# Kernel optimization log

Measured on AMD Instinct MI355X. Metric: run time of the kernel, lower is better.

The kernel has to match this reference:

```python
import jax, jax.numpy as jnp
import numpy as np

# Production-scale sampled 2-hop GraphSAGE flow
N, C, HID, OUT = 1_000_000, 128, 32, 16
NSRC1, NDST1, E1 = 600_000, 80_000, 1_280_000
NDST2, E2 = 8_000, 80_000


def setup_inputs() -> dict:
    key = jax.random.key(0)
    ks = jax.random.split(key, 8)
    x = jax.random.normal(ks[0], (N, C), jnp.float32)
    n_id = jax.random.randint(ks[1], (NSRC1,), 0, N)
    src1 = jax.random.randint(ks[2], (E1,), 0, NSRC1)
    dst1 = jax.random.randint(ks[3], (E1,), 0, NDST1)
    src2 = jax.random.randint(ks[4], (E2,), 0, NDST1)
    dst2 = jax.random.randint(ks[5], (E2,), 0, NDST2)
    W1 = jax.random.normal(ks[6], (C, HID), jnp.float32) / np.sqrt(C).astype(np.float32)
    b1 = jnp.zeros((HID,), jnp.float32)
    W2 = jax.random.normal(ks[7], (HID, OUT), jnp.float32) / np.sqrt(HID).astype(np.float32)
    b2 = jnp.zeros((OUT,), jnp.float32)
    return dict(x=x, n_id=n_id, src1=src1, dst1=dst1, src2=src2, dst2=dst2,
                W1=W1, b1=b1, W2=W2, b2=b2)


def _mean_agg(feat_src, src, dst, num_dst):
    # scatter-mean of source features onto destination nodes (PyG aggr='mean')
    msg = feat_src[src]                                          # [E, F]
    s = jax.ops.segment_sum(msg, dst, num_segments=num_dst)      # [num_dst, F]
    cnt = jax.ops.segment_sum(jnp.ones((src.shape[0],), feat_src.dtype), dst,
                              num_segments=num_dst)
    return s / jnp.maximum(cnt, 1.0)[:, None]


def reference(x, n_id, src1, dst1, src2, dst2, W1, b1, W2, b2):
    h = x[n_id]                                  # gather sampled nodes [NSRC1, C]
    # SAGEConv(concat=False, normalize=False): mean-agg then linear
    h = _mean_agg(h, src1, dst1, NDST1) @ W1 + b1
    h = jax.nn.relu(h)                           # F.dropout(p=0.5) is a no-op in eval
    h = _mean_agg(h, src2, dst2, NDST2) @ W2 + b2
    return jax.nn.log_softmax(h, axis=1)
```

## Files before the change

kernel.cpp:

```cpp
#include <hip/hip_runtime.h>
#include <hip/hip_fp16.h>
#include <math.h>

#define N_NODES  1000000
#define C_IN     128
#define HID      32
#define OUTF     16
#define NSRC1    600000
#define NDST1    80000
#define E1       1280000
#define NDST2    8000
#define E2       80000

#define KB1 4688
#define HB1 5000
#define HB2 313
#define AB1 313
#define AB2 32

#define T1A  1250
#define T1B  (KB1 - T1A)
#define GRP2 1719

#define K1_STRIDE 36

__device__ __forceinline__ void transform_body(
    const float* __restrict__ x, const int* __restrict__ n_id,
    const float* __restrict__ W1, __half* __restrict__ p,
    float* W_s, float (*A_t)[32 * K1_STRIDE], int idx)
{
    for (int i = threadIdx.x; i < C_IN * HID; i += 256) W_s[i] = W1[i];
    __syncthreads();

    const int wave = threadIdx.x >> 6;
    const int lane = threadIdx.x & 63;
    const int gwave = idx * 4 + wave;
    if (gwave >= NSRC1 / 32) return;
    const int s0 = gwave * 32;

    float* At = A_t[wave];

    int   mrow[4]; int f8[4]; const float* rowp[4];
    #pragma unroll
    for (int j = 0; j < 4; ++j) {
        int i2 = j * 64 + lane;
        mrow[j] = i2 >> 3;
        f8[j]   = i2 & 7;
        rowp[j] = x + (size_t)n_id[s0 + mrow[j]] * C_IN + f8[j] * 4;
    }

    const int m4 = lane >> 3;
    const int o4 = lane & 7;

    float acc[4][4];
    #pragma unroll
    for (int i = 0; i < 4; ++i)
        #pragma unroll
        for (int j = 0; j < 4; ++j) acc[i][j] = 0.f;

    float4 v[4];
    #pragma unroll
    for (int j = 0; j < 4; ++j) v[j] = *(const float4*)(rowp[j]);

    #pragma unroll
    for (int c = 0; c < 4; ++c) {
        #pragma unroll
        for (int j = 0; j < 4; ++j) {
            int kb = f8[j] * 4;
            int m  = mrow[j];
            At[(kb + 0) * K1_STRIDE + m] = v[j].x;
            At[(kb + 1) * K1_STRIDE + m] = v[j].y;
            At[(kb + 2) * K1_STRIDE + m] = v[j].z;
            At[(kb + 3) * K1_STRIDE + m] = v[j].w;
        }
        if (c < 3) {
            #pragma unroll
            for (int j = 0; j < 4; ++j)
                v[j] = *(const float4*)(rowp[j] + (c + 1) * 32);
        }
        #pragma unroll 4
        for (int k = 0; k < 32; ++k) {
            float4 a = *(const float4*)&At[k * K1_STRIDE + m4 * 4];
            float4 w = *(const float4*)&W_s[(c * 32 + k) * HID + o4 * 4];
            acc[0][0] += a.x * w.x; acc[0][1] += a.x * w.y; acc[0][2] += a.x * w.z; acc[0][3] += a.x * w.w;
            acc[1][0] += a.y * w.x; acc[1][1] += a.y * w.y; acc[1][2] += a.y * w.z; acc[1][3] += a.y * w.w;
            acc[2][0] += a.z * w.x; acc[2][1] += a.z * w.y; acc[2][2] += a.z * w.z; acc[2][3] += a.z * w.w;
            acc[3][0] += a.w * w.x; acc[3][1] += a.w * w.y; acc[3][2] += a.w * w.z; acc[3][3] += a.w * w.w;
        }
    }

    #pragma unroll
    for (int i = 0; i < 4; ++i) {
        union { __half2 h2[2]; uint2 u; } pk;
        pk.h2[0] = __floats2half2_rn(acc[i][0], acc[i][1]);
        pk.h2[1] = __floats2half2_rn(acc[i][2], acc[i][3]);
        *(uint2*)&p[(size_t)(s0 + m4 * 4 + i) * HID + o4 * 4] = pk.u;
    }
}

__global__ __launch_bounds__(256) void kA1_hist_transform(
    const float* __restrict__ x, const int* __restrict__ n_id,
    const float* __restrict__ W1, __half* __restrict__ p,
    const int* __restrict__ dst1, const int* __restrict__ dst2,
    int* __restrict__ deg1, int* __restrict__ deg2)
{
    __shared__ float W_s[C_IN * HID];
    __shared__ float A_t[4][32 * K1_STRIDE];

    const int bid = blockIdx.x;
    const int t = bid / 5, r = bid % 5;
    if (r == 0 && t < T1A) {
        transform_body(x, n_id, W1, p, W_s, A_t, t);
        return;
    }
    const int nt = min((bid + 4) / 5, T1A);
    const int h  = bid - nt;
    if (h < HB1) {
        int e = h * 256 + threadIdx.x;
        if (e < E1) atomicAdd(&deg1[dst1[e]], 1);
    } else {
        int e = (h - HB1) * 256 + threadIdx.x;
        if (e < E2) atomicAdd(&deg2[dst2[e]], 1);
    }
}

__global__ __launch_bounds__(256) void kB_alloc(
    const int* __restrict__ deg1, const int* __restrict__ deg2,
    int* __restrict__ rs1, int* __restrict__ rs2,
    int* __restrict__ cur1, int* __restrict__ cur2,
    int* __restrict__ counters)
{
    const int bid  = blockIdx.x;
    const int lane = threadIdx.x & 63;
    const int* deg; int* rs; int* cur; int* ctr; int nd; int d;
    if (bid < AB1) { deg = deg1; rs = rs1; cur = cur1; ctr = counters + 0;
                     nd = NDST1; d = bid * 256 + threadIdx.x; }
    else           { deg = deg2; rs = rs2; cur = cur2; ctr = counters + 1;
                     nd = NDST2; d = (bid - AB1) * 256 + threadIdx.x; }

    int v = (d < nd) ? deg[d] : 0;
    int incl = v;
    #pragma unroll
    for (int off = 1; off < 64; off <<= 1) {
        int t = __shfl_up(incl, off, 64);
        if (lane >= off) incl += t;
    }
    int total = __shfl(incl, 63, 64);
    int base = 0;
    if (lane == 63) base = atomicAdd(ctr, total);
    base = __shfl(base, 63, 64);
    if (d < nd) { int r = base + incl - v; rs[d] = r; cur[d] = r; }
}

__global__ __launch_bounds__(256) void kA2_bucket_transform(
    const float* __restrict__ x, const int* __restrict__ n_id,
    const float* __restrict__ W1, __half* __restrict__ p,
    const int* __restrict__ src1, const int* __restrict__ dst1,
    const int* __restrict__ src2, const int* __restrict__ dst2,
    int* __restrict__ cur1, int* __restrict__ cur2,
    int* __restrict__ ss1, int* __restrict__ ss2)
{
    __shared__ float W_s[C_IN * HID];
    __shared__ float A_t[4][32 * K1_STRIDE];

    const int bid = blockIdx.x;
    const int g = bid / 5, r = bid % 5;
    int bidx;
    if (g < GRP2) {
        if (r < 2) {
            int ti = 2 * g + r;
            if (ti < T1B) {
                transform_body(x, n_id, W1, p, W_s, A_t, T1A + ti);
                return;
            }
            bidx = 0;
        } else {
            bidx = 3 * g + (r - 2);
        }
    } else {
        bidx = 3 * GRP2 + (bid - 5 * GRP2);
    }

    if (bidx < HB1) {
        int e = bidx * 256 + threadIdx.x;
        if (e < E1) {
            int d = dst1[e];
            int pos = atomicAdd(&cur1[d], 1);
            ss1[pos] = src1[e];
        }
    } else {
        int e = (bidx - HB1) * 256 + threadIdx.x;
        if (e < E2) {
            int d = dst2[e];
            int pos = atomicAdd(&cur2[d], 1);
            ss2[pos] = src2[e];
        }
    }
}

__global__ __launch_bounds__(256) void kD_gather1(
    const int* __restrict__ row_start, const int* __restrict__ deg,
    const int* __restrict__ ss1, const __half* __restrict__ p,
    const float* __restrict__ b1, const float* __restrict__ W2,
    float* __restrict__ q)
{
    __shared__ float hbuf[16][HID + 1];
    const int g = threadIdx.x >> 4;
    const int f = threadIdx.x & 15;
    const int d = blockIdx.x * 16 + g;

    float w2r[HID];
    #pragma unroll
    for (int k = 0; k < HID; ++k) w2r[k] = W2[k * OUTF + f];
    const float2 b1v = *(const float2*)&b1[2 * f];

    const int start = row_start[d];
    const int dg    = deg[d];
    const __half2* ph2 = (const __half2*)p;

    float2 acc = make_float2(0.f, 0.f);
    int i = 0;
    for (; i + 4 <= dg; i += 4) {
        int s0 = ss1[start + i];
        int s1 = ss1[start + i + 1];
        int s2 = ss1[start + i + 2];
        int s3 = ss1[start + i + 3];
        float2 a = __half22float2(ph2[(size_t)s0 * 16 + f]);
        float2 b = __half22float2(ph2[(size_t)s1 * 16 + f]);
        float2 c = __half22float2(ph2[(size_t)s2 * 16 + f]);
        float2 e = __half22float2(ph2[(size_t)s3 * 16 + f]);
        acc.x += (a.x + b.x) + (c.x + e.x);
        acc.y += (a.y + b.y) + (c.y + e.y);
    }
    for (; i < dg; ++i) {
        float2 a = __half22float2(ph2[(size_t)ss1[start + i] * 16 + f]);
        acc.x += a.x; acc.y += a.y;
    }

    const float inv = 1.f / (float)max(dg, 1);
    hbuf[g][2 * f]     = fmaxf(acc.x * inv + b1v.x, 0.f);
    hbuf[g][2 * f + 1] = fmaxf(acc.y * inv + b1v.y, 0.f);
    float o = 0.f;
    #pragma unroll
    for (int k = 0; k < HID; ++k) o += hbuf[g][k] * w2r[k];
    q[(size_t)d * OUTF + f] = o;
}

__global__ __launch_bounds__(256) void kE_gather2_lsm(
    const int* __restrict__ row_start2, const int* __restrict__ deg2,
    const int* __restrict__ ss2, const float* __restrict__ q,
    const float* __restrict__ b2, float* __restrict__ out)
{
    const int g = threadIdx.x >> 4;
    const int f = threadIdx.x & 15;
    const int d = blockIdx.x * 16 + g;
    if (d >= NDST2) return;

    const int start = row_start2[d];
    const int dg    = deg2[d];

    float acc = 0.f;
    int i = 0;
    for (; i + 2 <= dg; i += 2) {
        int s0 = ss2[start + i];
        int s1 = ss2[start + i + 1];
        acc += q[(size_t)s0 * OUTF + f] + q[(size_t)s1 * OUTF + f];
    }
    if (i < dg) acc += q[(size_t)ss2[start + i] * OUTF + f];

    float z = acc / (float)max(dg, 1) + b2[f];
    float m = z;
    #pragma unroll
    for (int off = 8; off; off >>= 1) m = fmaxf(m, __shfl_xor(m, off, 16));
    float e = expf(z - m);
    float s = e;
    #pragma unroll
    for (int off = 8; off; off >>= 1) s += __shfl_xor(s, off, 16);
    out[(size_t)d * OUTF + f] = z - m - logf(s);
}

extern "C" void kernel_launch(void* const* d_in, const int* in_sizes, int n_in,
                              void* d_out, int out_size, void* d_ws, size_t ws_size,
                              hipStream_t stream)
{
    const float* x    = (const float*)d_in[0];
    const int*   n_id = (const int*)  d_in[1];
    const int*   src1 = (const int*)  d_in[2];
    const int*   dst1 = (const int*)  d_in[3];
    const int*   src2 = (const int*)  d_in[4];
    const int*   dst2 = (const int*)  d_in[5];
    const float* W1   = (const float*)d_in[6];
    const float* b1   = (const float*)d_in[7];
    const float* W2   = (const float*)d_in[8];
    const float* b2   = (const float*)d_in[9];
    float* out = (float*)d_out;

    char* ws = (char*)d_ws;
    __half* p       = (__half*)(ws + 0);
    int*   ss1      = (int*)   (ws + 38400000);
    int*   ss2      = (int*)   (ws + 43520000);
    int*   deg1     = (int*)   (ws + 43840000);
    int*   deg2     = (int*)   (ws + 44160000);
    int*   counters = (int*)   (ws + 44192000);
    int*   rs1      = (int*)   (ws + 44192064);
    int*   rs2      = (int*)   (ws + 44512064);
    int*   cur1     = (int*)   (ws + 44544064);
    int*   cur2     = (int*)   (ws + 44864064);
    float* q        = (float*) (ws + 44896064);

    hipMemsetAsync(deg1, 0, 352064, stream);

    kA1_hist_transform<<<T1A + HB1 + HB2, 256, 0, stream>>>(
        x, n_id, W1, p, dst1, dst2, deg1, deg2);

    kB_alloc<<<AB1 + AB2, 256, 0, stream>>>(deg1, deg2, rs1, rs2, cur1, cur2,
                                            counters);

    kA2_bucket_transform<<<T1B + HB1 + HB2, 256, 0, stream>>>(
        x, n_id, W1, p, src1, dst1, src2, dst2, cur1, cur2, ss1, ss2);

    kD_gather1<<<NDST1 / 16, 256, 0, stream>>>(rs1, deg1, ss1, p, b1, W2, q);

    kE_gather2_lsm<<<NDST2 / 16, 256, 0, stream>>>(rs2, deg2, ss2, q, b2, out);
}
```

Before: 754.8 us.

## Compute layer-1 transform with fp16 MFMA instead of scalar FMA via LDS

Replaces the scalar-FMA gather-transform (x[n_id] @ W1) with MFMA 16x16x32 f16 instructions. x rows are loaded directly into registers and converted to fp16, and W1 is pre-swizzled into fp16 in shared memory in the MFMA operand layout. This removes the LDS transpose staging and the large shared footprint, which should raise occupancy for the fused histogram and bucket kernels. The cost is reduced precision from the fp16 input and weight conversion.

Result: no change. 748.5 us (-0.8%).

```diff
diff --git a/kernel.cpp b/kernel.cpp
--- a/kernel.cpp
+++ b/kernel.cpp
@@ -22,14 +22,23 @@
 #define T1B  (KB1 - T1A)
 #define GRP2 1719
 
-#define K1_STRIDE 36
+typedef _Float16 f16x8 __attribute__((ext_vector_type(8)));
+typedef float    f32x4 __attribute__((ext_vector_type(4)));
 
 __device__ __forceinline__ void transform_body(
     const float* __restrict__ x, const int* __restrict__ n_id,
     const float* __restrict__ W1, __half* __restrict__ p,
-    float* W_s, float (*A_t)[32 * K1_STRIDE], int idx)
-{
-    for (int i = threadIdx.x; i < C_IN * HID; i += 256) W_s[i] = W1[i];
+    _Float16* W1f , int idx)
+{
+    for (int i = threadIdx.x; i < 4096; i += 256) {
+        int j  = i & 7;
+        int ln = (i >> 3) & 63;
+        int h  = (i >> 9) & 1;
+        int s  = i >> 10;
+        int k  = 32 * s + ((ln >> 4) << 3) + j;
+        int c  = (h << 4) + (ln & 15);
+        W1f[i] = (_Float16)W1[k * HID + c];
+    }
     __syncthreads();
 
     const int wave = threadIdx.x >> 6;
@@ -38,63 +47,61 @@
     if (gwave >= NSRC1 / 32) return;
     const int s0 = gwave * 32;
 
-    float* At = A_t[wave];
-
-    int   mrow[4]; int f8[4]; const float* rowp[4];
-    #pragma unroll
-    for (int j = 0; j < 4; ++j) {
-        int i2 = j * 64 + lane;
-        mrow[j] = i2 >> 3;
-        f8[j]   = i2 & 7;
-        rowp[j] = x + (size_t)n_id[s0 + mrow[j]] * C_IN + f8[j] * 4;
-    }
-
-    const int m4 = lane >> 3;
-    const int o4 = lane & 7;
-
-    float acc[4][4];
-    #pragma unroll
-    for (int i = 0; i < 4; ++i)
+    const int r15 = lane & 15;
+    const int q   = lane >> 4;
+
+    const float* xrow0 = x + (size_t)n_id[s0 + r15]      * C_IN + q * 8;
+    const float* xrow1 = x + (size_t)n_id[s0 + 16 + r15] * C_IN + q * 8;
+
+    float4 xf[2][4][2];
+    #pragma unroll
+    for (int s = 0; s < 4; ++s) {
+        xf[0][s][0] = *(const float4*)(xrow0 + 32 * s);
+        xf[0][s][1] = *(const float4*)(xrow0 + 32 * s + 4);
+        xf[1][s][0] = *(const float4*)(xrow1 + 32 * s);
+        xf[1][s][1] = *(const float4*)(xrow1 + 32 * s + 4);
+    }
+
+    f16x8 wf[4][2];
+    #pragma unroll
+    for (int s = 0; s < 4; ++s)
         #pragma unroll
-        for (int j = 0; j < 4; ++j) acc[i][j] = 0.f;
-
-    float4 v[4];
-    #pragma unroll
-    for (int j = 0; j < 4; ++j) v[j] = *(const float4*)(rowp[j]);
-
-    #pragma unroll
-    for (int c = 0; c < 4; ++c) {
+        for (int h = 0; h < 2; ++h)
+            wf[s][h] = *((const f16x8*)W1f + ((s * 2 + h) * 64 + lane));
+
+    f32x4 acc[2][2];
+    #pragma unroll
+    for (int mt = 0; mt < 2; ++mt)
         #pragma unroll
-        for (int j = 0; j < 4; ++j) {
-            int kb = f8[j] * 4;
-            int m  = mrow[j];
-            At[(kb + 0) * K1_STRIDE + m] = v[j].x;
-            At[(kb + 1) * K1_STRIDE + m] = v[j].y;
-            At[(kb + 2) * K1_STRIDE + m] = v[j].z;
-            At[(kb + 3) * K1_STRIDE + m] = v[j].w;
-        }
-        if (c < 3) {
+        for (int h = 0; h < 2; ++h)
+            acc[mt][h] = (f32x4){0.f, 0.f, 0.f, 0.f};
+
+    #pragma unroll
+    for (int mt = 0; mt < 2; ++mt) {
+        #pragma unroll
+        for (int s = 0; s < 4; ++s) {
+            f16x8 bf;
+            float4 lo = xf[mt][s][0], hi = xf[mt][s][1];
+            bf[0] = (_Float16)lo.x; bf[1] = (_Float16)lo.y;
+            bf[2] = (_Float16)lo.z; bf[3] = (_Float16)lo.w;
+            bf[4] = (_Float16)hi.x; bf[5] = (_Float16)hi.y;
+            bf[6] = (_Float16)hi.z; bf[7] = (_Float16)hi.w;
             #pragma unroll
-            for (int j = 0; j < 4; ++j)
-                v[j] = *(const float4*)(rowp[j] + (c + 1) * 32);
-        }
-        #pragma unroll 4
-        for (int k = 0; k < 32; ++k) {
-            float4 a = *(const float4*)&At[k * K1_STRIDE + m4 * 4];
-            float4 w = *(const float4*)&W_s[(c * 32 + k) * HID + o4 * 4];
-            acc[0][0] += a.x * w.x; acc[0][1] += a.x * w.y; acc[0][2] += a.x * w.z; acc[0][3] += a.x * w.w;
-            acc[1][0] += a.y * w.x; acc[1][1] += a.y * w.y; acc[1][2] += a.y * w.z; acc[1][3] += a.y * w.w;
-            acc[2][0] += a.z * w.x; acc[2][1] += a.z * w.y; acc[2][2] += a.z * w.z; acc[2][3] += a.z * w.w;
-            acc[3][0] += a.w * w.x; acc[3][1] += a.w * w.y; acc[3][2] += a.w * w.z; acc[3][3] += a.w * w.w;
-        }
-    }
-
-    #pragma unroll
-    for (int i = 0; i < 4; ++i) {
-        union { __half2 h2[2]; uint2 u; } pk;
-        pk.h2[0] = __floats2half2_rn(acc[i][0], acc[i][1]);
-        pk.h2[1] = __floats2half2_rn(acc[i][2], acc[i][3]);
-        *(uint2*)&p[(size_t)(s0 + m4 * 4 + i) * HID + o4 * 4] = pk.u;
+            for (int h = 0; h < 2; ++h)
+                acc[mt][h] = __builtin_amdgcn_mfma_f32_16x16x32_f16(
+                    wf[s][h], bf, acc[mt][h], 0, 0, 0);
+        }
+    }
+
+    #pragma unroll
+    for (int mt = 0; mt < 2; ++mt) {
+        #pragma unroll
+        for (int h = 0; h < 2; ++h) {
+            union { __half2 v[2]; uint2 u; } pk;
+            pk.v[0] = __floats2half2_rn(acc[mt][h][0], acc[mt][h][1]);
+            pk.v[1] = __floats2half2_rn(acc[mt][h][2], acc[mt][h][3]);
+            *(uint2*)&p[(size_t)(s0 + mt * 16 + r15) * HID + h * 16 + q * 4] = pk.u;
+        }
     }
 }
 
@@ -104,13 +111,12 @@
     const int* __restrict__ dst1, const int* __restrict__ dst2,
     int* __restrict__ deg1, int* __restrict__ deg2)
 {
-    __shared__ float W_s[C_IN * HID];
-    __shared__ float A_t[4][32 * K1_STRIDE];
+    __shared__ _Float16 W1f[4096];
 
     const int bid = blockIdx.x;
     const int t = bid / 5, r = bid % 5;
     if (r == 0 && t < T1A) {
-        transform_body(x, n_id, W1, p, W_s, A_t, t);
+        transform_body(x, n_id, W1, p, W1f, t);
         return;
     }
     const int nt = min((bid + 4) / 5, T1A);
@@ -160,8 +166,7 @@
     int* __restrict__ cur1, int* __restrict__ cur2,
     int* __restrict__ ss1, int* __restrict__ ss2)
 {
-    __shared__ float W_s[C_IN * HID];
-    __shared__ float A_t[4][32 * K1_STRIDE];
+    __shared__ _Float16 W1f[4096];
 
     const int bid = blockIdx.x;
     const int g = bid / 5, r = bid % 5;
@@ -170,7 +175,7 @@
         if (r < 2) {
             int ti = 2 * g + r;
             if (ti < T1B) {
-                transform_body(x, n_id, W1, p, W_s, A_t, T1A + ti);
+                transform_body(x, n_id, W1, p, W1f, T1A + ti);
                 return;
             }
             bidx = 0;
```
